# Optimization experiments

Hardware: AMD Instinct MI355X
Metric: run time of the kernel (lower is better)

## Reference

```python
import jax, jax.numpy as jnp
import numpy as np

WINDOW = 256  # sw_attention_window_size; query i attends to keys j with i-WINDOW <= j <= i


def setup_inputs() -> dict:
    key = jax.random.key(0)
    kq, kk, kv = jax.random.split(key, 3)
    shape = (4, 16, 4096, 64)  # [B, H, S, D]
    q = jax.random.normal(kq, shape, dtype=jnp.float32)
    k = jax.random.normal(kk, shape, dtype=jnp.float32)
    v = jax.random.normal(kv, shape, dtype=jnp.float32)
    return {"q": q, "k": k, "v": v}


def _local_attention(q, k, v, window):
    # Block-banded sliding-window attention: mask (j >= i - window) & (j <= i).
    # Uses block size == window so each query block only needs 2 key blocks.
    b, h, S, d = q.shape
    W = window
    T = S // W  # number of query blocks
    scale = jnp.asarray(d, q.dtype) ** -0.5  # flex_attention default scale

    qb = q.reshape(b, h, T, W, d)  # [b,h,T,W,d]

    def windows(x):
        # pad one block of zeros in front, then each query block t sees
        # key positions [t*W - W, t*W + W) == blocks (t, t+1) of the padded seq
        xp = jnp.pad(x, ((0, 0), (0, 0), (W, 0), (0, 0)))
        blk = xp.reshape(b, h, T + 1, W, d)
        return jnp.concatenate([blk[:, :, :-1], blk[:, :, 1:]], axis=3)  # [b,h,T,2W,d]

    kw = windows(k)
    vw = windows(v)

    # mask: global i = t*W + qi, global j = t*W - W + kj
    qi = jnp.arange(W)[:, None]          # [W,1]
    kj = jnp.arange(2 * W)[None, :]      # [1,2W]
    band = (kj >= qi) & (kj <= qi + W)   # i-W <= j <= i   -> [W,2W]
    t = jnp.arange(T)[:, None, None]     # [T,1,1]
    valid = (t * W - W + kj[None, :, :]) >= 0  # j >= 0 (drop padded keys)
    mask = band[None, :, :] & valid      # [T,W,2W]

    scores = jnp.einsum('bhtqd,bhtkd->bhtqk', qb, kw) * scale  # [b,h,T,W,2W]
    scores = jnp.where(mask[None, None], scores, -jnp.inf)
    attn = jax.nn.softmax(scores, axis=-1)
    out = jnp.einsum('bhtqk,bhtkd->bhtqd', attn, vw)
    return out.reshape(b, h, S, d)


def reference(q, k, v):
    return _local_attention(q, k, v, WINDOW)
```

## Files before the change

### kernel.cpp

```cpp
#include <hip/hip_runtime.h>

typedef __attribute__((ext_vector_type(8))) short bf16x8;
typedef __attribute__((ext_vector_type(4))) float f32x4;

#define L2E 1.44269504088896340736f

__device__ __forceinline__ unsigned pk2(float lo, float hi) {
    unsigned r;
    asm("v_cvt_pk_bf16_f32 %0, %1, %2" : "=v"(r) : "v"(lo), "v"(hi));
    return r;
}

constexpr int D_   = 64;
constexpr int SEQ  = 4096;
constexpr int MQ   = 128;
constexpr int CK   = 128;
constexpr int KSTR = 72;
constexpr int VSTR = 132;
constexpr int OSTR = 68;

constexpr int SMEM_BYTES = 35840;

__global__ __launch_bounds__(256, 3)
void swattn_kernel(const float* __restrict__ Qg, const float* __restrict__ Kg,
                   const float* __restrict__ Vg, float* __restrict__ Og)
{
    __shared__ __align__(16) char smem[SMEM_BYTES];
    unsigned short* k_lds = (unsigned short*)smem;
    unsigned short* v_lds = (unsigned short*)(smem + CK * KSTR * 2);
    float*          o_lds = (float*)smem;

    const int tid  = threadIdx.x;
    const int wv   = tid >> 6;
    const int lane = tid & 63;
    const int g    = lane >> 4;
    const int n    = lane & 15;

    const int bh = blockIdx.x & 63;
    const int qb = blockIdx.x >> 6;
    const size_t base = (size_t)bh * SEQ * D_;
    const int q0 = qb * MQ;

    bf16x8 qf[2][2];
    #pragma unroll
    for (int nt = 0; nt < 2; ++nt) {
        const float* qp = Qg + base + (size_t)(q0 + wv * 32 + nt * 16 + n) * D_;
        #pragma unroll
        for (int ks = 0; ks < 2; ++ks) {
            f32x4 a = *(const f32x4*)(qp + ks * 32 + g * 8);
            f32x4 b = *(const f32x4*)(qp + ks * 32 + g * 8 + 4);
            union { bf16x8 v; unsigned u[4]; } t;
            t.u[0] = pk2(a.x * 0.125f, a.y * 0.125f);
            t.u[1] = pk2(a.z * 0.125f, a.w * 0.125f);
            t.u[2] = pk2(b.x * 0.125f, b.y * 0.125f);
            t.u[3] = pk2(b.z * 0.125f, b.w * 0.125f);
            qf[nt][ks] = t.v;
        }
    }

    f32x4 o_ac[4][2];
    #pragma unroll
    for (int a = 0; a < 4; ++a)
        #pragma unroll
        for (int b = 0; b < 2; ++b)
            o_ac[a][b] = f32x4{0.f, 0.f, 0.f, 0.f};
    float m_r[2] = {-1e30f, -1e30f};
    float l_r[2] = {0.0f, 0.0f};

    #pragma unroll
    for (int ci = 0; ci < 3; ++ci) {
        const int cb = qb - 2 + ci;
        if (cb < 0) continue;

        __syncthreads();

        {
            const f32x4* kp = (const f32x4*)(Kg + base + (size_t)cb * CK * D_);
            #pragma unroll
            for (int i = 0; i < 8; ++i) {
                int idx = tid + 256 * i;
                int row = idx >> 4, c4 = idx & 15;
                f32x4 x = kp[idx];
                *(uint2*)&k_lds[row * KSTR + c4 * 4] =
                    make_uint2(pk2(x.x, x.y), pk2(x.z, x.w));
            }
        }
        {
            const f32x4* vp = (const f32x4*)(Vg + base + (size_t)cb * CK * D_);
            const int g16 = tid & 15, kq = tid >> 4;
            #pragma unroll
            for (int h = 0; h < 2; ++h) {
                int key0 = (kq + 16 * h) * 4;
                union { f32x4 v; float f[4]; } r0, r1, r2, r3;
                r0.v = vp[(key0 + 0) * 16 + g16];
                r1.v = vp[(key0 + 1) * 16 + g16];
                r2.v = vp[(key0 + 2) * 16 + g16];
                r3.v = vp[(key0 + 3) * 16 + g16];
                #pragma unroll
                for (int i = 0; i < 4; ++i) {
                    *(uint2*)&v_lds[(g16 * 4 + i) * VSTR + key0] =
                        make_uint2(pk2(r0.f[i], r1.f[i]), pk2(r2.f[i], r3.f[i]));
                }
            }
        }
        __syncthreads();

        f32x4 sc[8][2];
        #pragma unroll
        for (int mt = 0; mt < 8; ++mt)
            #pragma unroll
            for (int nt = 0; nt < 2; ++nt)
                sc[mt][nt] = f32x4{0.f, 0.f, 0.f, 0.f};

        __builtin_amdgcn_s_setprio(1);
        #pragma unroll
        for (int ks = 0; ks < 2; ++ks) {
            #pragma unroll
            for (int mt = 0; mt < 8; ++mt) {
                bf16x8 af = *(const bf16x8*)&k_lds[(mt * 16 + n) * KSTR + ks * 32 + g * 8];
                sc[mt][0] = __builtin_amdgcn_mfma_f32_16x16x32_bf16(af, qf[0][ks], sc[mt][0], 0, 0, 0);
                sc[mt][1] = __builtin_amdgcn_mfma_f32_16x16x32_bf16(af, qf[1][ks], sc[mt][1], 0, 0, 0);
            }
        }
        __builtin_amdgcn_s_setprio(0);

        if (ci != 1) {
            #pragma unroll
            for (int mt = 0; mt < 8; ++mt)
                #pragma unroll
                for (int nt = 0; nt < 2; ++nt)
                    #pragma unroll
                    for (int r = 0; r < 4; ++r) {
                        int kk = mt * 16 + g * 4 + r;
                        int qq = wv * 32 + nt * 16 + n;
                        bool ok = (ci == 0) ? (kk >= qq) : (kk <= qq);
                        if (!ok) sc[mt][nt][r] = -1e30f;
                    }
        }

        uint2 pkv[8][2];
        #pragma unroll
        for (int nt = 0; nt < 2; ++nt) {
            float t8[8];
            #pragma unroll
            for (int mt = 0; mt < 8; ++mt)
                t8[mt] = fmaxf(fmaxf(sc[mt][nt][0], sc[mt][nt][1]),
                               fmaxf(sc[mt][nt][2], sc[mt][nt][3]));
            float ma = fmaxf(t8[0], t8[1]), mb = fmaxf(t8[2], t8[3]);
            float mc = fmaxf(t8[4], t8[5]), md = fmaxf(t8[6], t8[7]);
            float mx = fmaxf(fmaxf(ma, mb), fmaxf(mc, md));
            mx = fmaxf(mx, __shfl_xor(mx, 16, 64));
            mx = fmaxf(mx, __shfl_xor(mx, 32, 64));
            float mnew = fmaxf(m_r[nt], mx);
            float al   = __builtin_amdgcn_exp2f((m_r[nt] - mnew) * L2E);
            m_r[nt] = mnew;
            float c  = -mnew * L2E;
            float s8[8];
            #pragma unroll
            for (int mt = 0; mt < 8; ++mt) {
                float p0 = __builtin_amdgcn_exp2f(fmaf(sc[mt][nt][0], L2E, c));
                float p1 = __builtin_amdgcn_exp2f(fmaf(sc[mt][nt][1], L2E, c));
                float p2 = __builtin_amdgcn_exp2f(fmaf(sc[mt][nt][2], L2E, c));
                float p3 = __builtin_amdgcn_exp2f(fmaf(sc[mt][nt][3], L2E, c));
                s8[mt] = (p0 + p1) + (p2 + p3);
                pkv[mt][nt] = make_uint2(pk2(p0, p1), pk2(p2, p3));
            }
            float ra = s8[0] + s8[1], rb = s8[2] + s8[3];
            float rc = s8[4] + s8[5], rd = s8[6] + s8[7];
            float rs = (ra + rb) + (rc + rd);
            rs += __shfl_xor(rs, 16, 64);
            rs += __shfl_xor(rs, 32, 64);
            l_r[nt] = l_r[nt] * al + rs;
            #pragma unroll
            for (int mtd = 0; mtd < 4; ++mtd)
                #pragma unroll
                for (int r = 0; r < 4; ++r)
                    o_ac[mtd][nt][r] *= al;
        }

        __builtin_amdgcn_s_setprio(1);
        #pragma unroll
        for (int kp4 = 0; kp4 < 4; ++kp4) {
            bf16x8 bfr[2];
            #pragma unroll
            for (int nt = 0; nt < 2; ++nt) {
                union { bf16x8 v; uint2 u2[2]; } bb;
                bb.u2[0] = pkv[2 * kp4][nt];
                bb.u2[1] = pkv[2 * kp4 + 1][nt];
                bfr[nt] = bb.v;
            }
            #pragma unroll
            for (int mtd = 0; mtd < 4; ++mtd) {
                int bus = (mtd * 16 + n) * VSTR + kp4 * 32 + g * 4;
                union { bf16x8 v; uint2 u2[2]; } aa;
                aa.u2[0] = *(const uint2*)&v_lds[bus];
                aa.u2[1] = *(const uint2*)&v_lds[bus + 16];
                o_ac[mtd][0] = __builtin_amdgcn_mfma_f32_16x16x32_bf16(aa.v, bfr[0], o_ac[mtd][0], 0, 0, 0);
                o_ac[mtd][1] = __builtin_amdgcn_mfma_f32_16x16x32_bf16(aa.v, bfr[1], o_ac[mtd][1], 0, 0, 0);
            }
        }
        __builtin_amdgcn_s_setprio(0);
    }

    __syncthreads();
    float inv[2] = {1.0f / l_r[0], 1.0f / l_r[1]};
    #pragma unroll
    for (int mtd = 0; mtd < 4; ++mtd)
        #pragma unroll
        for (int nt = 0; nt < 2; ++nt) {
            f32x4 v = o_ac[mtd][nt];
            v.x *= inv[nt]; v.y *= inv[nt]; v.z *= inv[nt]; v.w *= inv[nt];
            *(f32x4*)&o_lds[(wv * 32 + nt * 16 + n) * OSTR + mtd * 16 + g * 4] = v;
        }
    __syncthreads();

    f32x4* op = (f32x4*)(Og + base + (size_t)q0 * D_);
    #pragma unroll
    for (int p = 0; p < 8; ++p) {
        int row = p * 16 + (tid >> 4);
        int c4  = tid & 15;
        f32x4 v = *(const f32x4*)&o_lds[row * OSTR + c4 * 4];
        op[row * 16 + c4] = v;
    }
}

extern "C" void kernel_launch(void* const* d_in, const int* in_sizes, int n_in,
                              void* d_out, int out_size, void* d_ws, size_t ws_size,
                              hipStream_t stream) {
    (void)in_sizes; (void)n_in; (void)out_size; (void)d_ws; (void)ws_size;
    const float* q = (const float*)d_in[0];
    const float* k = (const float*)d_in[1];
    const float* v = (const float*)d_in[2];
    float* o = (float*)d_out;
    dim3 grid(64 * 32), block(256);
    hipLaunchKernelGGL(swattn_kernel, grid, block, 0, stream, q, k, v, o);
}
```

Measured before the change: 248.0 us.

## Process query subtiles sequentially per chunk to cut register pressure

Restructures the per-chunk loop so each wave handles its two 16-query subtiles one at a time: QK^T, masking, softmax and PV for one subtile finish before the next starts. This halves the live score and probability register arrays, and sched_barrier keeps the two subtiles apart. It also swaps launch_bounds min-blocks for an explicit waves_per_eu(3,3) hint to pin occupancy. In exchange, each K and V fragment is now read from LDS twice and there is less interleaved MFMA work to hide latency.

```diff
diff --git a/kernel.cpp b/kernel.cpp
--- a/kernel.cpp
+++ b/kernel.cpp
@@ -21,7 +21,7 @@
 
 constexpr int SMEM_BYTES = 35840;
 
-__global__ __launch_bounds__(256, 3)
+__global__ __launch_bounds__(256) __attribute__((amdgpu_waves_per_eu(3, 3)))
 void swattn_kernel(const float* __restrict__ Qg, const float* __restrict__ Kg,
                    const float* __restrict__ Vg, float* __restrict__ Og)
 {
@@ -40,6 +40,8 @@
     const int qb = blockIdx.x >> 6;
     const size_t base = (size_t)bh * SEQ * D_;
     const int q0 = qb * MQ;
+
+    const int g16 = tid & 15, kq = tid >> 4;
 
     bf16x8 qf[2][2];
     #pragma unroll
@@ -87,7 +89,6 @@
         }
         {
             const f32x4* vp = (const f32x4*)(Vg + base + (size_t)cb * CK * D_);
-            const int g16 = tid & 15, kq = tid >> 4;
             #pragma unroll
             for (int h = 0; h < 2; ++h) {
                 int key0 = (kq + 16 * h) * 4;
@@ -105,101 +106,94 @@
         }
         __syncthreads();
 
-        f32x4 sc[8][2];
-        #pragma unroll
-        for (int mt = 0; mt < 8; ++mt)
-            #pragma unroll
-            for (int nt = 0; nt < 2; ++nt)
-                sc[mt][nt] = f32x4{0.f, 0.f, 0.f, 0.f};
-
-        __builtin_amdgcn_s_setprio(1);
-        #pragma unroll
-        for (int ks = 0; ks < 2; ++ks) {
-            #pragma unroll
-            for (int mt = 0; mt < 8; ++mt) {
-                bf16x8 af = *(const bf16x8*)&k_lds[(mt * 16 + n) * KSTR + ks * 32 + g * 8];
-                sc[mt][0] = __builtin_amdgcn_mfma_f32_16x16x32_bf16(af, qf[0][ks], sc[mt][0], 0, 0, 0);
-                sc[mt][1] = __builtin_amdgcn_mfma_f32_16x16x32_bf16(af, qf[1][ks], sc[mt][1], 0, 0, 0);
-            }
-        }
-        __builtin_amdgcn_s_setprio(0);
-
-        if (ci != 1) {
+        #pragma unroll
+        for (int nt = 0; nt < 2; ++nt) {
+            f32x4 sc[8];
             #pragma unroll
             for (int mt = 0; mt < 8; ++mt)
-                #pragma unroll
-                for (int nt = 0; nt < 2; ++nt)
+                sc[mt] = f32x4{0.f, 0.f, 0.f, 0.f};
+
+            __builtin_amdgcn_s_setprio(1);
+            #pragma unroll
+            for (int ks = 0; ks < 2; ++ks) {
+                #pragma unroll
+                for (int mt = 0; mt < 8; ++mt) {
+                    bf16x8 af = *(const bf16x8*)&k_lds[(mt * 16 + n) * KSTR + ks * 32 + g * 8];
+                    sc[mt] = __builtin_amdgcn_mfma_f32_16x16x32_bf16(af, qf[nt][ks], sc[mt], 0, 0, 0);
+                }
+            }
+            __builtin_amdgcn_s_setprio(0);
+
+            if (ci != 1) {
+                #pragma unroll
+                for (int mt = 0; mt < 8; ++mt)
                     #pragma unroll
                     for (int r = 0; r < 4; ++r) {
                         int kk = mt * 16 + g * 4 + r;
                         int qq = wv * 32 + nt * 16 + n;
                         bool ok = (ci == 0) ? (kk >= qq) : (kk <= qq);
-                        if (!ok) sc[mt][nt][r] = -1e30f;
+                        if (!ok) sc[mt][r] = -1e30f;
                     }
-        }
-
-        uint2 pkv[8][2];
-        #pragma unroll
-        for (int nt = 0; nt < 2; ++nt) {
-            float t8[8];
-            #pragma unroll
-            for (int mt = 0; mt < 8; ++mt)
-                t8[mt] = fmaxf(fmaxf(sc[mt][nt][0], sc[mt][nt][1]),
-                               fmaxf(sc[mt][nt][2], sc[mt][nt][3]));
-            float ma = fmaxf(t8[0], t8[1]), mb = fmaxf(t8[2], t8[3]);
-            float mc = fmaxf(t8[4], t8[5]), md = fmaxf(t8[6], t8[7]);
-            float mx = fmaxf(fmaxf(ma, mb), fmaxf(mc, md));
-            mx = fmaxf(mx, __shfl_xor(mx, 16, 64));
-            mx = fmaxf(mx, __shfl_xor(mx, 32, 64));
-            float mnew = fmaxf(m_r[nt], mx);
-            float al   = __builtin_amdgcn_exp2f((m_r[nt] - mnew) * L2E);
-            m_r[nt] = mnew;
-            float c  = -mnew * L2E;
-            float s8[8];
-            #pragma unroll
-            for (int mt = 0; mt < 8; ++mt) {
-                float p0 = __builtin_amdgcn_exp2f(fmaf(sc[mt][nt][0], L2E, c));
-                float p1 = __builtin_amdgcn_exp2f(fmaf(sc[mt][nt][1], L2E, c));
-                float p2 = __builtin_amdgcn_exp2f(fmaf(sc[mt][nt][2], L2E, c));
-                float p3 = __builtin_amdgcn_exp2f(fmaf(sc[mt][nt][3], L2E, c));
-                s8[mt] = (p0 + p1) + (p2 + p3);
-                pkv[mt][nt] = make_uint2(pk2(p0, p1), pk2(p2, p3));
-            }
-            float ra = s8[0] + s8[1], rb = s8[2] + s8[3];
-            float rc = s8[4] + s8[5], rd = s8[6] + s8[7];
-            float rs = (ra + rb) + (rc + rd);
-            rs += __shfl_xor(rs, 16, 64);
-            rs += __shfl_xor(rs, 32, 64);
-            l_r[nt] = l_r[nt] * al + rs;
-            #pragma unroll
-            for (int mtd = 0; mtd < 4; ++mtd)
-                #pragma unroll
-                for (int r = 0; r < 4; ++r)
-                    o_ac[mtd][nt][r] *= al;
-        }
-
-        __builtin_amdgcn_s_setprio(1);
-        #pragma unroll
-        for (int kp4 = 0; kp4 < 4; ++kp4) {
-            bf16x8 bfr[2];
-            #pragma unroll
-            for (int nt = 0; nt < 2; ++nt) {
+            }
+
+            uint2 pkv[8];
+            {
+                float t8[8];
+                #pragma unroll
+                for (int mt = 0; mt < 8; ++mt)
+                    t8[mt] = fmaxf(fmaxf(sc[mt][0], sc[mt][1]),
+                                   fmaxf(sc[mt][2], sc[mt][3]));
+                float ma = fmaxf(t8[0], t8[1]), mb = fmaxf(t8[2], t8[3]);
+                float mc = fmaxf(t8[4], t8[5]), md = fmaxf(t8[6], t8[7]);
+                float mx = fmaxf(fmaxf(ma, mb), fmaxf(mc, md));
+                mx = fmaxf(mx, __shfl_xor(mx, 16, 64));
+                mx = fmaxf(mx, __shfl_xor(mx, 32, 64));
+                float mnew = fmaxf(m_r[nt], mx);
+                float al   = __builtin_amdgcn_exp2f((m_r[nt] - mnew) * L2E);
+                m_r[nt] = mnew;
+                float c  = -mnew * L2E;
+                float s8[8];
+                #pragma unroll
+                for (int mt = 0; mt < 8; ++mt) {
+                    float p0 = __builtin_amdgcn_exp2f(fmaf(sc[mt][0], L2E, c));
+                    float p1 = __builtin_amdgcn_exp2f(fmaf(sc[mt][1], L2E, c));
+                    float p2 = __builtin_amdgcn_exp2f(fmaf(sc[mt][2], L2E, c));
+                    float p3 = __builtin_amdgcn_exp2f(fmaf(sc[mt][3], L2E, c));
+                    s8[mt] = (p0 + p1) + (p2 + p3);
+                    pkv[mt] = make_uint2(pk2(p0, p1), pk2(p2, p3));
+                }
+                float ra = s8[0] + s8[1], rb = s8[2] + s8[3];
+                float rc = s8[4] + s8[5], rd = s8[6] + s8[7];
+                float rs = (ra + rb) + (rc + rd);
+                rs += __shfl_xor(rs, 16, 64);
+                rs += __shfl_xor(rs, 32, 64);
+                l_r[nt] = l_r[nt] * al + rs;
+                #pragma unroll
+                for (int mtd = 0; mtd < 4; ++mtd)
+                    #pragma unroll
+                    for (int r = 0; r < 4; ++r)
+                        o_ac[mtd][nt][r] *= al;
+            }
+
+            __builtin_amdgcn_s_setprio(1);
+            #pragma unroll
+            for (int kp4 = 0; kp4 < 4; ++kp4) {
                 union { bf16x8 v; uint2 u2[2]; } bb;
-                bb.u2[0] = pkv[2 * kp4][nt];
-                bb.u2[1] = pkv[2 * kp4 + 1][nt];
-                bfr[nt] = bb.v;
-            }
-            #pragma unroll
-            for (int mtd = 0; mtd < 4; ++mtd) {
-                int bus = (mtd * 16 + n) * VSTR + kp4 * 32 + g * 4;
-                union { bf16x8 v; uint2 u2[2]; } aa;
-                aa.u2[0] = *(const uint2*)&v_lds[bus];
-                aa.u2[1] = *(const uint2*)&v_lds[bus + 16];
-                o_ac[mtd][0] = __builtin_amdgcn_mfma_f32_16x16x32_bf16(aa.v, bfr[0], o_ac[mtd][0], 0, 0, 0);
-                o_ac[mtd][1] = __builtin_amdgcn_mfma_f32_16x16x32_bf16(aa.v, bfr[1], o_ac[mtd][1], 0, 0, 0);
-            }
-        }
-        __builtin_amdgcn_s_setprio(0);
+                bb.u2[0] = pkv[2 * kp4];
+                bb.u2[1] = pkv[2 * kp4 + 1];
+                #pragma unroll
+                for (int mtd = 0; mtd < 4; ++mtd) {
+                    int bus = (mtd * 16 + n) * VSTR + kp4 * 32 + g * 4;
+                    union { bf16x8 v; uint2 u2[2]; } aa;
+                    aa.u2[0] = *(const uint2*)&v_lds[bus];
+                    aa.u2[1] = *(const uint2*)&v_lds[bus + 16];
+                    o_ac[mtd][nt] = __builtin_amdgcn_mfma_f32_16x16x32_bf16(aa.v, bb.v, o_ac[mtd][nt], 0, 0, 0);
+                }
+            }
+            __builtin_amdgcn_s_setprio(0);
+
+            __builtin_amdgcn_sched_barrier(0);
+        }
     }
 
     __syncthreads();
```

New measurement: 323.5 us. 30.4% more time.
